# Performance work log

Measured on AMD Instinct MI355X. Metric: run time of the kernel, lower is better.

Reference implementation:

```python
import jax, jax.numpy as jnp
import numpy as np
from jax.scipy.special import logsumexp

WORD_DIM = 512
SCRF_DIM = 256
N_TAGS = 12
ALLOWED_SPAN = 8
START_ID = 10
STOP_ID = 11
SEQ_LEN = 768
N_SPANS = 96


def _compute_scores(h, Wl, bl, Wr, br, Gl, bgl, Gr, bgr, Wt, bt, transitions):
    # h: [1, L, D] already projected by Dense
    Lc, D = h.shape[1], h.shape[2]
    scores = jnp.zeros((1, Lc, Lc, D), h.dtype)
    diag = jnp.arange(Lc)
    ht = h
    scores = scores.at[:, diag, diag].set(ht)
    for sl in range(1, min(ALLOWED_SPAN, Lc)):
        l, r = ht[:, :-1], ht[:, 1:]
        h_hat = 4.0 * jax.nn.sigmoid(l @ Wl.T + bl + r @ Wr.T + br) - 2.0
        # exp/normalize over 3 gates == softmax over gate axis
        g = (l @ Gl.T + bgl + r @ Gr.T + bgr).reshape(1, Lc - sl, 3, D)
        wgt = jax.nn.softmax(g, axis=2)
        ht = wgt[:, :, 0] * h_hat + wgt[:, :, 1] * l + wgt[:, :, 2] * r
        scores = scores.at[:, diag[:Lc - sl], diag[sl:]].set(ht)
    tagsc = scores @ Wt.T + bt  # [1, L, L, T]
    # final[b,i,j,prev,tag] = tagsc[b,i,j,tag] + transitions[prev,tag]
    return tagsc[:, :, :, None, :] + transitions[None, None, None]


def _forward_pass(s5):
    # s5: [1, L, L, T, T]; semi-Markov forward algorithm, windows of width <= ALLOWED_SPAN
    Lc, T = s5.shape[1], s5.shape[3]
    A = ALLOWED_SPAN
    i0 = jnp.arange(1, Lc + 1)
    k = jnp.arange(A)
    p = i0[:, None] - A + k[None, :]              # candidate span-start positions [L, A]
    m = p >= 0                                    # valid window mask (istarts = max(0, i-A))
    x = s5[0][jnp.clip(p, 0), (i0 - 1)[:, None]]  # [L, A, T, T] span scores ending at i-1
    buf0 = jnp.full((A, T), -10000.0, s5.dtype).at[A - 1, START_ID].set(0.0)

    def step(buf, inp):
        xi, mi = inp
        # tmp[k, prev, tag] = score + logalpha[start, prev]
        tmp = jnp.where(mi[:, None, None], xi + buf[:, :, None], -1e30)
        na = logsumexp(tmp, axis=(0, 1))  # [T]
        return jnp.concatenate([buf[1:], na[None]], axis=0), na

    _, alphas = jax.lax.scan(step, buf0, (x, m))
    return alphas[-1, :STOP_ID].sum()


def _gold_score(s5, tags):
    Lc, T = s5.shape[1], s5.shape[3]
    gf = tags[:, :, 0] * (Lc * T * T) + tags[:, :, 1] * (T * T) + tags[:, :, 2] * T + tags[:, :, 3]
    return jnp.take_along_axis(s5.reshape(1, -1), gf, axis=1).sum()


def setup_inputs() -> dict:
    key = jax.random.key(0)
    ks = jax.random.split(key, 16)
    D, W3 = SCRF_DIM, 3 * SCRF_DIM
    s = 0.05
    def w(k, shape):
        return jax.random.normal(k, shape, dtype=jnp.float32) * s
    return {
        "feats": jax.random.normal(ks[0], (1, SEQ_LEN, WORD_DIM), dtype=jnp.float32),
        "tags": jax.random.randint(ks[1], (1, N_SPANS, 4), 0, N_TAGS),
        "Wd": w(ks[2], (D, WORD_DIM)), "bd": jnp.zeros((D,), jnp.float32),
        "Wl": w(ks[3], (D, D)), "bl": jnp.zeros((D,), jnp.float32),
        "Wr": w(ks[4], (D, D)), "br": jnp.zeros((D,), jnp.float32),
        "Gl": w(ks[5], (W3, D)), "bgl": jnp.zeros((W3,), jnp.float32),
        "Gr": w(ks[6], (W3, D)), "bgr": jnp.zeros((W3,), jnp.float32),
        "Wt": w(ks[7], (N_TAGS, D)), "bt": jnp.zeros((N_TAGS,), jnp.float32),
        "transitions": w(ks[8], (N_TAGS, N_TAGS)),
    }


def reference(feats, tags, Wd, bd, Wl, bl, Wr, br, Gl, bgl, Gr, bgr, Wt, bt, transitions):
    h = feats @ Wd.T + bd  # Dense: word_dim -> scrf_dim
    s5 = _compute_scores(h, Wl, bl, Wr, br, Gl, bgl, Gr, bgr, Wt, bt, transitions)
    gold = _gold_score(s5, tags)
    logZ = _forward_pass(s5)
    return logZ - gold
```

## Files before the change

kernel.cpp:

```cpp
#include <hip/hip_runtime.h>

typedef __attribute__((ext_vector_type(8))) short short8;
typedef __attribute__((ext_vector_type(4))) float f32x4;

#define TPAD 100

__device__ __forceinline__ float bf2f(short s) {
  return __uint_as_float(((unsigned)(unsigned short)s) << 16);
}
__device__ __forceinline__ unsigned short f2bf(float f) {
  unsigned u = __float_as_uint(f);
  unsigned rounding = 0x7fffu + ((u >> 16) & 1u);
  return (unsigned short)((u + rounding) >> 16);
}

__device__ __forceinline__ void stg_f32(float* p, float v) {
  asm volatile("global_store_dword %0, %1, off sc1" :: "v"(p), "v"(v) : "memory");
}
__device__ __forceinline__ void stg_u16(unsigned short* p, unsigned short v) {
  unsigned w = v;
  asm volatile("global_store_short %0, %1, off sc1" :: "v"(p), "v"(w) : "memory");
}
__device__ __forceinline__ void stg_u32(unsigned* p, unsigned v) {
  asm volatile("global_store_dword %0, %1, off sc1" :: "v"(p), "v"(v) : "memory");
}

#define NFLAGS 18432
__device__ __forceinline__ void flag_spin(unsigned* f, unsigned tgt) {
  unsigned n = 0;
  while (__hip_atomic_load(f, __ATOMIC_RELAXED, __HIP_MEMORY_SCOPE_AGENT) < tgt) {
    __builtin_amdgcn_s_sleep(1);
    if (++n > 2000000u) break;
  }
}
#define DRAIN() asm volatile("s_waitcnt vmcnt(0) lgkmcnt(0)" ::: "memory")

union __align__(16) SmemU {
  struct { unsigned short As[64][72]; unsigned short Ws[64][72]; float Cs[64][64]; } g;
  struct { unsigned short rows[2][8][264]; float sred[2][96]; float smu[2]; } bn;
  struct { float Bs[96 * TPAD]; float Acs[96 * TPAD]; float red[8]; } t;
  struct { float Qs[2][96 * TPAD]; float vv[4][96]; float red[8]; float redm[4]; } f;
};

__global__ void prep_kernel(const float* __restrict__ feats, const float* __restrict__ Wd,
                            const float* __restrict__ Wl, const float* __restrict__ Wr,
                            const float* __restrict__ Gl, const float* __restrict__ Gr,
                            const float* __restrict__ bl, const float* __restrict__ br,
                            const float* __restrict__ bgl, const float* __restrict__ bgr,
                            unsigned short* __restrict__ featsB, unsigned short* __restrict__ WdB,
                            unsigned short* __restrict__ WcB, float* __restrict__ bc,
                            unsigned* __restrict__ flags)
{
  int idx = blockIdx.x * 256 + threadIdx.x;
  if (idx < 393216) {
    featsB[idx] = f2bf(feats[idx]);
  } else if (idx < 524288) {
    int j = idx - 393216;
    WdB[j] = f2bf(Wd[j]);
  } else if (idx < 1048576) {
    int j = idx - 524288;
    int o = j >> 9, k = j & 511;
    float v;
    if (k < 256) v = (o < 256) ? Wl[o*256 + k] : Gl[(o-256)*256 + k];
    else { int k2 = k - 256; v = (o < 256) ? Wr[o*256 + k2] : Gr[(o-256)*256 + k2]; }
    WcB[j] = f2bf(v);
  } else if (idx < 1049600) {
    int o = idx - 1048576;
    bc[o] = (o < 256) ? bl[o] + br[o] : bgl[o-256] + bgr[o-256];
  } else {
    int j = idx - 1049600;
    if (j < NFLAGS) flags[j] = 0u;
  }
}

__device__ __forceinline__ void treelevel(SmemU& sm,
    const float* Tin, const float* Cin, float* Tout, float* Cout)
{
  const int bid = blockIdx.x;
  const int tid = threadIdx.x;
  const int wv = tid >> 6, lane = tid & 63;
  const int j = bid >> 1;
  const int cs = (bid & 1) * 48;
  const float* Ag = Tin + (size_t)(2*j) * 9216;
  const float* Bg = Tin + (size_t)(2*j + 1) * 9216;

  float4 av[9], bv[9];
  const float* ap = Ag + tid * 36;
  const float* bp = Bg + tid * 36;
  #pragma unroll
  for (int q = 0; q < 9; ++q) av[q] = *(const float4*)(ap + q*4);
  #pragma unroll
  for (int q = 0; q < 9; ++q) bv[q] = *(const float4*)(bp + q*4);
  float ma = 0.f, mb = 0.f;
  #pragma unroll
  for (int q = 0; q < 9; ++q) {
    ma = fmaxf(ma, fmaxf(fmaxf(av[q].x, av[q].y), fmaxf(av[q].z, av[q].w)));
    mb = fmaxf(mb, fmaxf(fmaxf(bv[q].x, bv[q].y), fmaxf(bv[q].z, bv[q].w)));
  }
  #pragma unroll
  for (int off = 32; off; off >>= 1) {
    ma = fmaxf(ma, __shfl_down(ma, off));
    mb = fmaxf(mb, __shfl_down(mb, off));
  }
  if (lane == 0) { sm.t.red[wv] = ma; sm.t.red[4 + wv] = mb; }
  __syncthreads();
  float fa = fmaxf(fmaxf(sm.t.red[0], sm.t.red[1]), fmaxf(sm.t.red[2], sm.t.red[3]));
  float fb = fmaxf(fmaxf(sm.t.red[4], sm.t.red[5]), fmaxf(sm.t.red[6], sm.t.red[7]));
  float ia = 1.0f / fa, ib = 1.0f / fb;

  #pragma unroll
  for (int q = 0; q < 9; ++q) {
    int e = tid*36 + q*4;
    int r = e / 96, k = e - r*96;
    float4 bb = bv[q];
    bb.x *= ib; bb.y *= ib; bb.z *= ib; bb.w *= ib;
    *(float4*)&sm.t.Bs[r*TPAD + k] = bb;
    float4 aa = av[q];
    sm.t.Acs[(k+0)*TPAD + r] = aa.x * ia;
    sm.t.Acs[(k+1)*TPAD + r] = aa.y * ia;
    sm.t.Acs[(k+2)*TPAD + r] = aa.z * ia;
    sm.t.Acs[(k+3)*TPAD + r] = aa.w * ia;
  }
  __syncthreads();

  int tr = tid >> 4, tc = tid & 15;
  int r0 = tr * 6, c0 = cs + tc * 3;
  float acc[6][3];
  #pragma unroll
  for (int i = 0; i < 6; ++i)
    #pragma unroll
    for (int m = 0; m < 3; ++m) acc[i][m] = 0.f;
  for (int k = 0; k < 96; k += 4) {
    float4 a0 = *(const float4*)&sm.t.Acs[(c0+0)*TPAD + k];
    float4 a1 = *(const float4*)&sm.t.Acs[(c0+1)*TPAD + k];
    float4 a2 = *(const float4*)&sm.t.Acs[(c0+2)*TPAD + k];
    #pragma unroll
    for (int i = 0; i < 6; ++i) {
      float4 b = *(const float4*)&sm.t.Bs[(r0+i)*TPAD + k];
      acc[i][0] += b.x*a0.x + b.y*a0.y + b.z*a0.z + b.w*a0.w;
      acc[i][1] += b.x*a1.x + b.y*a1.y + b.z*a1.z + b.w*a1.w;
      acc[i][2] += b.x*a2.x + b.y*a2.y + b.z*a2.z + b.w*a2.w;
    }
  }
  float* op = Tout + (size_t)j * 9216;
  #pragma unroll
  for (int i = 0; i < 6; ++i)
    #pragma unroll
    for (int m = 0; m < 3; ++m)
      stg_f32(&op[(size_t)(r0+i)*96 + c0 + m], acc[i][m]);
  if ((bid & 1) == 0 && tid == 0)
    stg_f32(&Cout[j], Cin[2*j] + Cin[2*j + 1] + __logf(fa) + __logf(fb));
}

__global__ __launch_bounds__(256, 2) void mega_kernel(
    const unsigned short* featsB, const unsigned short* WdB,
    const float* bd, const unsigned short* WcB, const float* bc,
    unsigned short* ht, const float* Wt, const float* bt,
    float* Bband, float* Xn, float* muv, const float* trans,
    const int* tags,
    float* T0, float* T1, float* T2, float* T3, float* T4,
    float* C0, float* C1, float* C2, float* C3, float* C4,
    float* out, unsigned* flags)
{
  __shared__ SmemU sm;
  const int bid = blockIdx.x;
  const int tid = threadIdx.x;
  const int wave = tid >> 6, lane = tid & 63;

  if (bid < 192) {
    const int p = bid % 12;
    const int lr = tid >> 3;
    const int c8 = (tid & 7) * 8;
    if (bid < 48) {
      const int p0 = p * 64;
      const int n0 = (bid / 12) * 64;
      f32x4 acc[4];
      #pragma unroll
      for (int i = 0; i < 4; ++i)
        #pragma unroll
        for (int j = 0; j < 4; ++j) acc[i][j] = 0.f;
      short8 a0r, a1r, w0r, w1r;
      a0r = *(const short8*)(featsB + (size_t)(p0 + lr)*512 + c8);
      a1r = *(const short8*)(featsB + (size_t)(p0 + lr + 32)*512 + c8);
      w0r = *(const short8*)(WdB + (size_t)(n0 + lr)*512 + c8);
      w1r = *(const short8*)(WdB + (size_t)(n0 + lr + 32)*512 + c8);
      for (int kt = 0; kt < 8; ++kt) {
        *(short8*)(&sm.g.As[lr][c8])      = a0r;
        *(short8*)(&sm.g.As[lr + 32][c8]) = a1r;
        *(short8*)(&sm.g.Ws[lr][c8])      = w0r;
        *(short8*)(&sm.g.Ws[lr + 32][c8]) = w1r;
        __syncthreads();
        if (kt < 7) {
          int kb = (kt + 1) * 64;
          a0r = *(const short8*)(featsB + (size_t)(p0 + lr)*512 + kb + c8);
          a1r = *(const short8*)(featsB + (size_t)(p0 + lr + 32)*512 + kb + c8);
          w0r = *(const short8*)(WdB + (size_t)(n0 + lr)*512 + kb + c8);
          w1r = *(const short8*)(WdB + (size_t)(n0 + lr + 32)*512 + kb + c8);
        }
        int q8 = (lane >> 4) * 8;
        #pragma unroll
        for (int kk = 0; kk < 2; ++kk) {
          short8 bfr = *(const short8*)(&sm.g.Ws[wave*16 + (lane & 15)][kk*32 + q8]);
          #pragma unroll
          for (int mt = 0; mt < 4; ++mt) {
            short8 afr = *(const short8*)(&sm.g.As[mt*16 + (lane & 15)][kk*32 + q8]);
            acc[mt] = __builtin_amdgcn_mfma_f32_16x16x32_bf16(afr, bfr, acc[mt], 0, 0, 0);
          }
        }
        __syncthreads();
      }
      int o = n0 + wave*16 + (lane & 15);
      float bias = bd[o];
      #pragma unroll
      for (int mt = 0; mt < 4; ++mt)
        #pragma unroll
        for (int r = 0; r < 4; ++r) {
          int row = p0 + mt*16 + (lane >> 4)*4 + r;
          stg_u16(&ht[row*256 + o], f2bf(acc[mt][r] + bias));
        }
      DRAIN();
      __syncthreads();
      if (tid == 0) atomicAdd(&flags[(0*12 + p)*32], 1u);
    }

    const int p0 = p * 64;
    const int n0i = (bid / 12) * 16;
    for (int sl = 1; sl <= 7; ++sl) {
      short8 w0r, w1r, a0r, a1r;
      {
        int o0 = (lr >> 4)*256 + n0i + (lr & 15);
        int o1 = ((lr+32) >> 4)*256 + n0i + ((lr+32) & 15);
        w0r = *(const short8*)(WcB + (size_t)o0*512 + c8);
        w1r = *(const short8*)(WcB + (size_t)o1*512 + c8);
      }
      unsigned tgt = (sl == 1) ? 4u : 16u;
      if (tid == 0) {
        flag_spin(&flags[((sl-1)*12 + p)*32], tgt);
        if (p < 11) flag_spin(&flags[((sl-1)*12 + p + 1)*32], tgt);
      }
      __syncthreads();
      {
        const unsigned short* htp = ht + (size_t)(sl - 1) * 196608;
        unsigned short* htn = ht + (size_t)sl * 196608;
        const int Mvalid = 768 - sl;
        f32x4 acc[4];
        #pragma unroll
        for (int i = 0; i < 4; ++i)
          #pragma unroll
          for (int j = 0; j < 4; ++j) acc[i][j] = 0.f;
        {
          int g0 = p0 + lr;      if (g0 > 767) g0 = 767;
          int g1 = p0 + lr + 32; if (g1 > 767) g1 = 767;
          a0r = *(const short8*)(htp + (size_t)g0*256 + c8);
          a1r = *(const short8*)(htp + (size_t)g1*256 + c8);
        }
        for (int kt = 0; kt < 8; ++kt) {
          *(short8*)(&sm.g.As[lr][c8])      = a0r;
          *(short8*)(&sm.g.As[lr + 32][c8]) = a1r;
          *(short8*)(&sm.g.Ws[lr][c8])      = w0r;
          *(short8*)(&sm.g.Ws[lr + 32][c8]) = w1r;
          __syncthreads();
          if (kt < 7) {
            int kb = (kt + 1) * 64;
            int shift = kb >> 8;
            int kcol = kb & 255;
            int g0 = p0 + lr + shift;      if (g0 > 767) g0 = 767;
            int g1 = p0 + lr + 32 + shift; if (g1 > 767) g1 = 767;
            a0r = *(const short8*)(htp + (size_t)g0*256 + kcol + c8);
            a1r = *(const short8*)(htp + (size_t)g1*256 + kcol + c8);
            int o0 = (lr >> 4)*256 + n0i + (lr & 15);
            int o1 = ((lr+32) >> 4)*256 + n0i + ((lr+32) & 15);
            w0r = *(const short8*)(WcB + (size_t)o0*512 + kb + c8);
            w1r = *(const short8*)(WcB + (size_t)o1*512 + kb + c8);
          }
          int q8 = (lane >> 4) * 8;
          #pragma unroll
          for (int kk = 0; kk < 2; ++kk) {
            short8 bfr = *(const short8*)(&sm.g.Ws[wave*16 + (lane & 15)][kk*32 + q8]);
            #pragma unroll
            for (int mt = 0; mt < 4; ++mt) {
              short8 afr = *(const short8*)(&sm.g.As[mt*16 + (lane & 15)][kk*32 + q8]);
              acc[mt] = __builtin_amdgcn_mfma_f32_16x16x32_bf16(afr, bfr, acc[mt], 0, 0, 0);
            }
          }
          __syncthreads();
        }
        #pragma unroll
        for (int mt = 0; mt < 4; ++mt)
          #pragma unroll
          for (int r = 0; r < 4; ++r)
            sm.g.Cs[mt*16 + (lane >> 4)*4 + r][wave*16 + (lane & 15)] = acc[mt][r];
        __syncthreads();

        int dl = tid & 7;
        int d0 = n0i + dl*2;
        int cc0 = dl*2;
        float bz0 = bc[d0],       bz1 = bc[d0+1];
        float b00 = bc[256 + d0], b01 = bc[256 + d0 + 1];
        float b10 = bc[512 + d0], b11 = bc[512 + d0 + 1];
        float b20 = bc[768 + d0], b21 = bc[768 + d0 + 1];
        for (int pr = tid >> 3; pr < 64; pr += 32) {
          int pw = p0 + pr;
          if (pw >= Mvalid) continue;
          float z0 = sm.g.Cs[pr][cc0]      + bz0, z1 = sm.g.Cs[pr][cc0+1]      + bz1;
          float g00 = sm.g.Cs[pr][16+cc0]  + b00, g01 = sm.g.Cs[pr][16+cc0+1]  + b01;
          float g10 = sm.g.Cs[pr][32+cc0]  + b10, g11 = sm.g.Cs[pr][32+cc0+1]  + b11;
          float g20 = sm.g.Cs[pr][48+cc0]  + b20, g21 = sm.g.Cs[pr][48+cc0+1]  + b21;
          unsigned lv = *(const unsigned*)(htp + (size_t)pw*256 + d0);
          unsigned rv = *(const unsigned*)(htp + (size_t)(pw+1)*256 + d0);
          float l0 = bf2f((short)(lv & 0xffff)), l1 = bf2f((short)(lv >> 16));
          float r0v = bf2f((short)(rv & 0xffff)), r1v = bf2f((short)(rv >> 16));
          float hh0 = 4.f / (1.f + __expf(-z0)) - 2.f;
          float hh1 = 4.f / (1.f + __expf(-z1)) - 2.f;
          float mg0 = fmaxf(g00, fmaxf(g10, g20));
          float mg1 = fmaxf(g01, fmaxf(g11, g21));
          float e00 = __expf(g00 - mg0), e10 = __expf(g10 - mg0), e20 = __expf(g20 - mg0);
          float e01 = __expf(g01 - mg1), e11 = __expf(g11 - mg1), e21 = __expf(g21 - mg1);
          float o0 = (e00*hh0 + e10*l0 + e20*r0v) / (e00 + e10 + e20);
          float o1 = (e01*hh1 + e11*l1 + e21*r1v) / (e01 + e11 + e21);
          unsigned pack = (unsigned)f2bf(o0) | ((unsigned)f2bf(o1) << 16);
          stg_u32((unsigned*)(htn + (size_t)pw*256 + d0), pack);
        }
      }
      DRAIN();
      __syncthreads();
      if (tid == 0) atomicAdd(&flags[(sl*12 + p)*32], 1u);
    }
  }

  for (int task = bid; task < 384; task += 256) {
    if (tid == 0) {
      int rlo = 2*task - 7; if (rlo < 0) rlo = 0;
      int tlo = rlo >> 6, thi = (2*task + 1) >> 6;
      flag_spin(&flags[(7*12 + tlo)*32], 16u);
      if (thi != tlo) flag_spin(&flags[(7*12 + thi)*32], 16u);
    }
    __syncthreads();
    const int half = tid >> 7;
    const int t2 = tid & 127;
    const int i = 2*task + 1 + half;
    for (int q = t2; q < 256; q += 128) {
      int k = q >> 5, cc = (q & 31) * 8;
      int pr = i - 8 + k;
      short8 v;
      if (pr >= 0) {
        int slx = 7 - k;
        v = *(const short8*)(ht + ((size_t)slx*768 + pr)*256 + cc);
      } else {
        #pragma unroll
        for (int j = 0; j < 8; ++j) v[j] = 0;
      }
      *(short8*)(&sm.bn.rows[half][k][cc]) = v;
    }
    __syncthreads();
    float res = -1e30f;
    if (t2 < 96) {
      int t = t2 >> 3, k = t2 & 7;
      int pr = i - 8 + k;
      if (pr >= 0) {
        float acc = 0.f;
        for (int dch = 0; dch < 256; dch += 8) {
          float4 wa = *(const float4*)(Wt + t*256 + dch);
          float4 wb = *(const float4*)(Wt + t*256 + dch + 4);
          short8 hv = *(const short8*)(&sm.bn.rows[half][k][dch]);
          acc += wa.x*bf2f(hv[0]) + wa.y*bf2f(hv[1]) + wa.z*bf2f(hv[2]) + wa.w*bf2f(hv[3])
               + wb.x*bf2f(hv[4]) + wb.y*bf2f(hv[5]) + wb.z*bf2f(hv[6]) + wb.w*bf2f(hv[7]);
        }
        res = acc + bt[t];
      }
      stg_f32(&Bband[(size_t)i*96 + t2], res);
      sm.bn.sred[half][t2] = res;
    }
    __syncthreads();
    if (t2 < 32) {
      float m = fmaxf(sm.bn.sred[half][t2],
                 fmaxf(sm.bn.sred[half][t2+32], sm.bn.sred[half][t2+64]));
      #pragma unroll
      for (int off = 16; off; off >>= 1) m = fmaxf(m, __shfl_down(m, off));
      if (t2 == 0) { stg_f32(&muv[i], m); sm.bn.smu[half] = m; }
    }
    __syncthreads();
    if (t2 < 96) stg_f32(&Xn[(size_t)i*96 + t2], __expf(res - sm.bn.smu[half]));
    DRAIN();
    __syncthreads();
    if (tid == 0) atomicAdd(&flags[(96 + task)*32], 1u);
  }
  if (bid >= 240) return;

  {
    const int chunk = bid / 5;
    const int bxx = bid % 5;
    if (tid == 0) {
      #pragma unroll
      for (int q = 0; q < 8; ++q)
        flag_spin(&flags[(96 + 8*chunk + q)*32], 1u);
    }
    __syncthreads();
    if (bxx == 0 && tid == 0) stg_f32(&C0[chunk], 0.f);
    const int a = chunk * 16;
    const int g = lane / 12;
    const int t = lane - g * 12;
    const int cidx = bxx * 20 + wave * 5 + g;
    const bool active = (g < 5) && (cidx < 96);
    const int c = active ? cidx : 95;
    const int s = c / 12, tau = c - s * 12;
    float Etc[12];
    #pragma unroll
    for (int jj = 0; jj < 12; ++jj) Etc[jj] = __expf(trans[jj*12 + t]);
    float NA[8], V[8];
    #pragma unroll
    for (int jj = 0; jj < 8; ++jj) { NA[jj] = 0.f; V[jj] = 0.f; }
    #pragma unroll
    for (int jj = 0; jj < 8; ++jj) if (jj == s) {
      NA[jj] = (t == tau) ? 1.f : 0.f;
      V[jj]  = Etc[tau];
    }
    const int gbb = (g * 12) * 4;
    #pragma unroll
    for (int m = 1; m <= 16; ++m) {
      const float* xr = Xn + (size_t)(a + m) * 96 + t * 8;
      float4 x0 = *(const float4*)xr;
      float4 x1 = *(const float4*)(xr + 4);
      float sf = __expf(-muv[a + m]);
      float na = x0.x*V[0] + x0.y*V[1] + x0.z*V[2] + x0.w*V[3]
               + x1.x*V[4] + x1.y*V[5] + x1.z*V[6] + x1.w*V[7];
      int nai = __float_as_int(na);
      float nb[12];
      #pragma unroll
      for (int jj = 0; jj < 12; ++jj)
        nb[jj] = __int_as_float(__builtin_amdgcn_ds_bpermute(gbb + jj*4, nai));
      float pp0 = nb[0]*Etc[0] + nb[1]*Etc[1] + nb[2]*Etc[2]   + nb[3]*Etc[3];
      float pp1 = nb[4]*Etc[4] + nb[5]*Etc[5] + nb[6]*Etc[6]   + nb[7]*Etc[7];
      float pp2 = nb[8]*Etc[8] + nb[9]*Etc[9] + nb[10]*Etc[10] + nb[11]*Etc[11];
      float v = (pp0 + pp1) + pp2;
      #pragma unroll
      for (int kq = 0; kq < 7; ++kq) { NA[kq] = NA[kq+1]*sf; V[kq] = V[kq+1]*sf; }
      NA[7] = na; V[7] = v;
    }
    if (active) {
      float* dst = T0 + (size_t)chunk * 9216 + c;
      #pragma unroll
      for (int jj = 0; jj < 8; ++jj) stg_f32(&dst[(size_t)(jj*12 + t) * 96], NA[jj]);
    }
    DRAIN();
    __syncthreads();
    if (tid == 0) atomicAdd(&flags[(480 + chunk)*32], 1u);
  }
  if (bid >= 48) return;

  {
    int j = bid >> 1;
    if (tid == 0) {
      flag_spin(&flags[(480 + 2*j    )*32], 5u);
      flag_spin(&flags[(480 + 2*j + 1)*32], 5u);
    }
    __syncthreads();
    treelevel(sm, T0, C0, T1, C1);
    DRAIN(); __syncthreads();
    if (tid == 0) atomicAdd(&flags[(528 + j)*32], 1u);
  }
  if (bid >= 24) return;
  {
    int j = bid >> 1;
    if (tid == 0) {
      flag_spin(&flags[(528 + 2*j    )*32], 2u);
      flag_spin(&flags[(528 + 2*j + 1)*32], 2u);
    }
    __syncthreads();
    treelevel(sm, T1, C1, T2, C2);
    DRAIN(); __syncthreads();
    if (tid == 0) atomicAdd(&flags[(552 + j)*32], 1u);
  }
  if (bid >= 12) return;
  {
    int j = bid >> 1;
    if (tid == 0) {
      flag_spin(&flags[(552 + 2*j    )*32], 2u);
      flag_spin(&flags[(552 + 2*j + 1)*32], 2u);
    }
    __syncthreads();
    treelevel(sm, T2, C2, T3, C3);
    DRAIN(); __syncthreads();
    if (tid == 0) atomicAdd(&flags[(564 + j)*32], 1u);
  }
  if (bid >= 6) return;
  {
    int j = bid >> 1;
    if (tid == 0) {
      flag_spin(&flags[(564 + 2*j    )*32], 2u);
      flag_spin(&flags[(564 + 2*j + 1)*32], 2u);
    }
    __syncthreads();
    treelevel(sm, T3, C3, T4, C4);
    DRAIN(); __syncthreads();
    if (tid == 0) atomicAdd(&flags[(570 + j)*32], 1u);
  }
  if (bid) return;

  {
    if (tid == 0) {
      flag_spin(&flags[(570)*32], 2u);
      flag_spin(&flags[(571)*32], 2u);
      flag_spin(&flags[(572)*32], 2u);
    }
    __syncthreads();
    float4 P[9];
    const float* p0p = T4 + tid * 36;
    #pragma unroll
    for (int q = 0; q < 9; ++q) P[q] = *(const float4*)(p0p + q*4);

    float gold = 0.f;
    if (tid < 96) {
      int a = tags[tid*4+0], b = tags[tid*4+1], cc = tags[tid*4+2], d = tags[tid*4+3];
      float v = trans[cc*12 + d];
      int sl = b - a;
      if (sl >= 0 && sl < 8) v += Bband[(size_t)(b+1)*96 + d*8 + (7 - sl)];
      else v += bt[d];
      gold = v;
    }
    float mp = 0.f;
    for (int q = tid; q < 768; q += 256) mp += muv[1 + q];
    #pragma unroll
    for (int off = 32; off; off >>= 1) {
      gold += __shfl_down(gold, off);
      mp   += __shfl_down(mp, off);
    }
    if (lane == 0) { sm.f.red[wave] = gold; sm.f.red[4 + wave] = mp; }

    #pragma unroll
    for (int q = 0; q < 9; ++q) {
      int e = tid*36 + q*4;
      int r = e / 96, k = e - r*96;
      *(float4*)&sm.f.Qs[0][r*TPAD + k] = P[q];
    }
    if (tid < 96) sm.f.vv[0][tid] = (tid == 94) ? 1.f : 0.f;
    __syncthreads();
    float gold_t = sm.f.red[0] + sm.f.red[1] + sm.f.red[2] + sm.f.red[3];
    float musum  = sm.f.red[4] + sm.f.red[5] + sm.f.red[6] + sm.f.red[7];
    float Ct = C4[0] + C4[1] + C4[2];

    #pragma unroll
    for (int s = 0; s < 3; ++s) {
      if (s < 2) {
        const float* pn = T4 + (size_t)(s+1)*9216 + tid*36;
        #pragma unroll
        for (int q = 0; q < 9; ++q) P[q] = *(const float4*)(pn + q*4);
      }
      float acc = 0.f;
      if (tid < 96) {
        const float* Qr = &sm.f.Qs[s & 1][tid * TPAD];
        #pragma unroll
        for (int k = 0; k < 96; k += 4) {
          float4 qv = *(const float4*)(Qr + k);
          float4 zv = *(const float4*)&sm.f.vv[s][k];
          acc += qv.x*zv.x + qv.y*zv.y + qv.z*zv.z + qv.w*zv.w;
        }
      }
      float am = (tid < 96) ? acc : 0.f;
      #pragma unroll
      for (int off = 32; off; off >>= 1) am = fmaxf(am, __shfl_down(am, off));
      if (lane == 0) sm.f.redm[wave] = am;
      __syncthreads();
      float mx = fmaxf(fmaxf(sm.f.redm[0], sm.f.redm[1]), fmaxf(sm.f.redm[2], sm.f.redm[3]));
      Ct += __logf(mx);
      if (tid < 96) sm.f.vv[s+1][tid] = acc / mx;
      if (s < 2) {
        #pragma unroll
        for (int q = 0; q < 9; ++q) {
          int e = tid*36 + q*4;
          int r = e / 96, k = e - r*96;
          *(float4*)&sm.f.Qs[(s+1)&1][r*TPAD + k] = P[q];
        }
      }
      __syncthreads();
    }
    if (tid == 0) {
      float lsum = 0.f;
      #pragma unroll
      for (int t = 0; t < 11; ++t) lsum += __logf(sm.f.vv[3][84 + t]);
      out[0] = lsum + 11.f * (Ct + musum) - gold_t;
    }
  }
}

extern "C" void kernel_launch(void* const* d_in, const int* in_sizes, int n_in,
                              void* d_out, int out_size, void* d_ws, size_t ws_size,
                              hipStream_t stream)
{
  const float* feats = (const float*)d_in[0];
  const int*   tags  = (const int*)  d_in[1];
  const float* Wd    = (const float*)d_in[2];
  const float* bd    = (const float*)d_in[3];
  const float* Wl    = (const float*)d_in[4];
  const float* bl    = (const float*)d_in[5];
  const float* Wr    = (const float*)d_in[6];
  const float* br    = (const float*)d_in[7];
  const float* Gl    = (const float*)d_in[8];
  const float* bgl   = (const float*)d_in[9];
  const float* Gr    = (const float*)d_in[10];
  const float* bgr   = (const float*)d_in[11];
  const float* Wt    = (const float*)d_in[12];
  const float* bt    = (const float*)d_in[13];
  const float* trans = (const float*)d_in[14];
  float* out = (float*)d_out;

  char* ws = (char*)d_ws;
  unsigned short* featsB = (unsigned short*)(ws + 0);
  unsigned short* WdB    = (unsigned short*)(ws + 786432);
  unsigned short* WcB    = (unsigned short*)(ws + 1048576);
  float*          bc     = (float*)         (ws + 2097152);
  unsigned short* ht     = (unsigned short*)(ws + 2101248);
  float*          Bband  = (float*)         (ws + 5246976);
  float*          Xn     = (float*)         (ws + 5542272);
  float*          muv    = (float*)         (ws + 5837568);
  float*          T0     = (float*)         (ws + 5841664);
  float*          T1     = (float*)         (ws + 7611136);
  float*          T2     = (float*)         (ws + 8495872);
  float*          T3     = (float*)         (ws + 8938240);
  float*          T4     = (float*)         (ws + 9159424);
  float*          C0     = (float*)         (ws + 9270016);
  float*          C1     = (float*)         (ws + 9270272);
  float*          C2     = (float*)         (ws + 9270528);
  float*          C3     = (float*)         (ws + 9270784);
  float*          C4     = (float*)         (ws + 9271040);
  unsigned*       flags  = (unsigned*)      (ws + 9271296);

  prep_kernel<<<4172, 256, 0, stream>>>(feats, Wd, Wl, Wr, Gl, Gr, bl, br, bgl, bgr,
                                        featsB, WdB, WcB, bc, flags);
  mega_kernel<<<256, 256, 0, stream>>>(featsB, WdB, bd, WcB, bc, ht, Wt, bt,
                                       Bband, Xn, muv, trans, tags,
                                       T0, T1, T2, T3, T4, C0, C1, C2, C3, C4,
                                       out, flags);
}
```

Baseline: 211.6 us.

## Fuse bf16 conversion into mega kernel and double-buffer GEMM LDS tiles

Drops the feats/Wd bf16 pre-conversion from the prep kernel: the projection GEMM now loads fp32 inputs and converts them in registers, and blocks 48+ build the combined WcB weight inside the mega kernel, with a flag that the span GEMMs wait on. Both GEMM loops get double-buffered LDS tiles, a two-stage register prefetch, and a lighter barrier macro. This removes most of the prep kernel's work and one global round trip, and overlaps loads with MFMA. In exchange it adds a new cross-block dependency through a spin flag, doubles the LDS tile footprint, and lowers launch bounds to one block per CU.

```diff
diff --git a/kernel.cpp b/kernel.cpp
--- a/kernel.cpp
+++ b/kernel.cpp
@@ -12,6 +12,17 @@
   unsigned u = __float_as_uint(f);
   unsigned rounding = 0x7fffu + ((u >> 16) & 1u);
   return (unsigned short)((u + rounding) >> 16);
+}
+
+struct F8 { float4 a, b; };
+__device__ __forceinline__ F8 ldf8(const float* p) {
+  F8 r; r.a = *(const float4*)p; r.b = *(const float4*)(p + 4); return r;
+}
+__device__ __forceinline__ short8 cvtF8(F8 v) {
+  short8 r;
+  r[0]=(short)f2bf(v.a.x); r[1]=(short)f2bf(v.a.y); r[2]=(short)f2bf(v.a.z); r[3]=(short)f2bf(v.a.w);
+  r[4]=(short)f2bf(v.b.x); r[5]=(short)f2bf(v.b.y); r[6]=(short)f2bf(v.b.z); r[7]=(short)f2bf(v.b.w);
+  return r;
 }
 
 __device__ __forceinline__ void stg_f32(float* p, float v) {
@@ -34,41 +45,28 @@
   }
 }
 #define DRAIN() asm volatile("s_waitcnt vmcnt(0) lgkmcnt(0)" ::: "memory")
+#define KTBAR() do { \
+  asm volatile("s_waitcnt lgkmcnt(0)" ::: "memory"); \
+  __builtin_amdgcn_s_barrier(); \
+  __builtin_amdgcn_sched_barrier(0); \
+} while (0)
 
 union __align__(16) SmemU {
-  struct { unsigned short As[64][72]; unsigned short Ws[64][72]; float Cs[64][64]; } g;
+  struct { unsigned short As[2][64][72]; unsigned short Ws[2][64][72]; float Cs[64][64]; } g;
   struct { unsigned short rows[2][8][264]; float sred[2][96]; float smu[2]; } bn;
   struct { float Bs[96 * TPAD]; float Acs[96 * TPAD]; float red[8]; } t;
   struct { float Qs[2][96 * TPAD]; float vv[4][96]; float red[8]; float redm[4]; } f;
 };
 
-__global__ void prep_kernel(const float* __restrict__ feats, const float* __restrict__ Wd,
-                            const float* __restrict__ Wl, const float* __restrict__ Wr,
-                            const float* __restrict__ Gl, const float* __restrict__ Gr,
-                            const float* __restrict__ bl, const float* __restrict__ br,
+__global__ void prep_kernel(const float* __restrict__ bl, const float* __restrict__ br,
                             const float* __restrict__ bgl, const float* __restrict__ bgr,
-                            unsigned short* __restrict__ featsB, unsigned short* __restrict__ WdB,
-                            unsigned short* __restrict__ WcB, float* __restrict__ bc,
-                            unsigned* __restrict__ flags)
+                            float* __restrict__ bc, unsigned* __restrict__ flags)
 {
   int idx = blockIdx.x * 256 + threadIdx.x;
-  if (idx < 393216) {
-    featsB[idx] = f2bf(feats[idx]);
-  } else if (idx < 524288) {
-    int j = idx - 393216;
-    WdB[j] = f2bf(Wd[j]);
-  } else if (idx < 1048576) {
-    int j = idx - 524288;
-    int o = j >> 9, k = j & 511;
-    float v;
-    if (k < 256) v = (o < 256) ? Wl[o*256 + k] : Gl[(o-256)*256 + k];
-    else { int k2 = k - 256; v = (o < 256) ? Wr[o*256 + k2] : Gr[(o-256)*256 + k2]; }
-    WcB[j] = f2bf(v);
-  } else if (idx < 1049600) {
-    int o = idx - 1048576;
-    bc[o] = (o < 256) ? bl[o] + br[o] : bgl[o-256] + bgr[o-256];
+  if (idx < 1024) {
+    bc[idx] = (idx < 256) ? bl[idx] + br[idx] : bgl[idx-256] + bgr[idx-256];
   } else {
-    int j = idx - 1049600;
+    int j = idx - 1024;
     if (j < NFLAGS) flags[j] = 0u;
   }
 }
@@ -152,9 +150,10 @@
     stg_f32(&Cout[j], Cin[2*j] + Cin[2*j + 1] + __logf(fa) + __logf(fb));
 }
 
-__global__ __launch_bounds__(256, 2) void mega_kernel(
-    const unsigned short* featsB, const unsigned short* WdB,
-    const float* bd, const unsigned short* WcB, const float* bc,
+__global__ __launch_bounds__(256, 1) void mega_kernel(
+    const float* feats, const float* Wd, const float* bd,
+    const float* Wl, const float* Wr, const float* Gl, const float* Gr,
+    unsigned short* WcB, const float* bc,
     unsigned short* ht, const float* Wt, const float* bt,
     float* Bband, float* Xn, float* muv, const float* trans,
     const int* tags,
@@ -167,6 +166,19 @@
   const int tid = threadIdx.x;
   const int wave = tid >> 6, lane = tid & 63;
 
+  if (bid >= 48) {
+    for (int j = (bid - 48)*256 + tid; j < 524288; j += 208*256) {
+      int o = j >> 9, k = j & 511;
+      float v;
+      if (k < 256) v = (o < 256) ? Wl[o*256 + k] : Gl[(o-256)*256 + k];
+      else { int k2 = k - 256; v = (o < 256) ? Wr[o*256 + k2] : Gr[(o-256)*256 + k2]; }
+      stg_u16(&WcB[j], f2bf(v));
+    }
+    DRAIN();
+    __syncthreads();
+    if (tid == 0) atomicAdd(&flags[573*32], 1u);
+  }
+
   if (bid < 192) {
     const int p = bid % 12;
     const int lr = tid >> 3;
@@ -179,35 +191,41 @@
       for (int i = 0; i < 4; ++i)
         #pragma unroll
         for (int j = 0; j < 4; ++j) acc[i][j] = 0.f;
-      short8 a0r, a1r, w0r, w1r;
-      a0r = *(const short8*)(featsB + (size_t)(p0 + lr)*512 + c8);
-      a1r = *(const short8*)(featsB + (size_t)(p0 + lr + 32)*512 + c8);
-      w0r = *(const short8*)(WdB + (size_t)(n0 + lr)*512 + c8);
-      w1r = *(const short8*)(WdB + (size_t)(n0 + lr + 32)*512 + c8);
+      F8 fa0[2], fa1[2], fw0[2], fw1[2];
+      #pragma unroll
+      for (int q = 0; q < 2; ++q) {
+        int kb = q * 64;
+        fa0[q] = ldf8(feats + (size_t)(p0 + lr)*512 + kb + c8);
+        fa1[q] = ldf8(feats + (size_t)(p0 + lr + 32)*512 + kb + c8);
+        fw0[q] = ldf8(Wd + (size_t)(n0 + lr)*512 + kb + c8);
+        fw1[q] = ldf8(Wd + (size_t)(n0 + lr + 32)*512 + kb + c8);
+      }
+      #pragma unroll
       for (int kt = 0; kt < 8; ++kt) {
-        *(short8*)(&sm.g.As[lr][c8])      = a0r;
-        *(short8*)(&sm.g.As[lr + 32][c8]) = a1r;
-        *(short8*)(&sm.g.Ws[lr][c8])      = w0r;
-        *(short8*)(&sm.g.Ws[lr + 32][c8]) = w1r;
-        __syncthreads();
-        if (kt < 7) {
-          int kb = (kt + 1) * 64;
-          a0r = *(const short8*)(featsB + (size_t)(p0 + lr)*512 + kb + c8);
-          a1r = *(const short8*)(featsB + (size_t)(p0 + lr + 32)*512 + kb + c8);
-          w0r = *(const short8*)(WdB + (size_t)(n0 + lr)*512 + kb + c8);
-          w1r = *(const short8*)(WdB + (size_t)(n0 + lr + 32)*512 + kb + c8);
-        }
+        const int sb = kt & 1;
+        *(short8*)(&sm.g.As[sb][lr][c8])      = cvtF8(fa0[sb]);
+        *(short8*)(&sm.g.As[sb][lr + 32][c8]) = cvtF8(fa1[sb]);
+        *(short8*)(&sm.g.Ws[sb][lr][c8])      = cvtF8(fw0[sb]);
+        *(short8*)(&sm.g.Ws[sb][lr + 32][c8]) = cvtF8(fw1[sb]);
+        if (kt < 6) {
+          int kb = (kt + 2) * 64;
+          fa0[sb] = ldf8(feats + (size_t)(p0 + lr)*512 + kb + c8);
+          fa1[sb] = ldf8(feats + (size_t)(p0 + lr + 32)*512 + kb + c8);
+          fw0[sb] = ldf8(Wd + (size_t)(n0 + lr)*512 + kb + c8);
+          fw1[sb] = ldf8(Wd + (size_t)(n0 + lr + 32)*512 + kb + c8);
+        }
+        KTBAR();
         int q8 = (lane >> 4) * 8;
         #pragma unroll
         for (int kk = 0; kk < 2; ++kk) {
-          short8 bfr = *(const short8*)(&sm.g.Ws[wave*16 + (lane & 15)][kk*32 + q8]);
+          short8 bfr = *(const short8*)(&sm.g.Ws[sb][wave*16 + (lane & 15)][kk*32 + q8]);
           #pragma unroll
           for (int mt = 0; mt < 4; ++mt) {
-            short8 afr = *(const short8*)(&sm.g.As[mt*16 + (lane & 15)][kk*32 + q8]);
+            short8 afr = *(const short8*)(&sm.g.As[sb][mt*16 + (lane & 15)][kk*32 + q8]);
             acc[mt] = __builtin_amdgcn_mfma_f32_16x16x32_bf16(afr, bfr, acc[mt], 0, 0, 0);
           }
         }
-        __syncthreads();
+        KTBAR();
       }
       int o = n0 + wave*16 + (lane & 15);
       float bias = bd[o];
@@ -225,13 +243,19 @@
 
     const int p0 = p * 64;
     const int n0i = (bid / 12) * 16;
+    const int o0w = (lr >> 4)*256 + n0i + (lr & 15);
+    const int o1w = ((lr+32) >> 4)*256 + n0i + ((lr+32) & 15);
     for (int sl = 1; sl <= 7; ++sl) {
-      short8 w0r, w1r, a0r, a1r;
-      {
-        int o0 = (lr >> 4)*256 + n0i + (lr & 15);
-        int o1 = ((lr+32) >> 4)*256 + n0i + ((lr+32) & 15);
-        w0r = *(const short8*)(WcB + (size_t)o0*512 + c8);
-        w1r = *(const short8*)(WcB + (size_t)o1*512 + c8);
+      if (sl == 1) {
+        if (tid == 0) flag_spin(&flags[573*32], 208u);
+        __syncthreads();
+      }
+      short8 sw0[2], sw1[2], sa0[2], sa1[2];
+      #pragma unroll
+      for (int q = 0; q < 2; ++q) {
+        int kb = q * 64;
+        sw0[q] = *(const short8*)(WcB + (size_t)o0w*512 + kb + c8);
+        sw1[q] = *(const short8*)(WcB + (size_t)o1w*512 + kb + c8);
       }
       unsigned tgt = (sl == 1) ? 4u : 16u;
       if (tid == 0) {
@@ -248,42 +272,44 @@
         for (int i = 0; i < 4; ++i)
           #pragma unroll
           for (int j = 0; j < 4; ++j) acc[i][j] = 0.f;
-        {
+        #pragma unroll
+        for (int q = 0; q < 2; ++q) {
+          int kb = q * 64;
           int g0 = p0 + lr;      if (g0 > 767) g0 = 767;
           int g1 = p0 + lr + 32; if (g1 > 767) g1 = 767;
-          a0r = *(const short8*)(htp + (size_t)g0*256 + c8);
-          a1r = *(const short8*)(htp + (size_t)g1*256 + c8);
-        }
+          sa0[q] = *(const short8*)(htp + (size_t)g0*256 + kb + c8);
+          sa1[q] = *(const short8*)(htp + (size_t)g1*256 + kb + c8);
+        }
+        #pragma unroll
         for (int kt = 0; kt < 8; ++kt) {
-          *(short8*)(&sm.g.As[lr][c8])      = a0r;
-          *(short8*)(&sm.g.As[lr + 32][c8]) = a1r;
-          *(short8*)(&sm.g.Ws[lr][c8])      = w0r;
-          *(short8*)(&sm.g.Ws[lr + 32][c8]) = w1r;
-          __syncthreads();
-          if (kt < 7) {
-            int kb = (kt + 1) * 64;
+          const int sb = kt & 1;
+          *(short8*)(&sm.g.As[sb][lr][c8])      = sa0[sb];
+          *(short8*)(&sm.g.As[sb][lr + 32][c8]) = sa1[sb];
+          *(short8*)(&sm.g.Ws[sb][lr][c8])      = sw0[sb];
+          *(short8*)(&sm.g.Ws[sb][lr + 32][c8]) = sw1[sb];
+          if (kt < 6) {
+            int kb = (kt + 2) * 64;
             int shift = kb >> 8;
             int kcol = kb & 255;
             int g0 = p0 + lr + shift;      if (g0 > 767) g0 = 767;
             int g1 = p0 + lr + 32 + shift; if (g1 > 767) g1 = 767;
-            a0r = *(const short8*)(htp + (size_t)g0*256 + kcol + c8);
-            a1r = *(const short8*)(htp + (size_t)g1*256 + kcol + c8);
-            int o0 = (lr >> 4)*256 + n0i + (lr & 15);
-            int o1 = ((lr+32) >> 4)*256 + n0i + ((lr+32) & 15);
-            w0r = *(const short8*)(WcB + (size_t)o0*512 + kb + c8);
-            w1r = *(const short8*)(WcB + (size_t)o1*512 + kb + c8);
+            sa0[sb] = *(const short8*)(htp + (size_t)g0*256 + kcol + c8);
+            sa1[sb] = *(const short8*)(htp + (size_t)g1*256 + kcol + c8);
+            sw0[sb] = *(const short8*)(WcB + (size_t)o0w*512 + kb + c8);
+            sw1[sb] = *(const short8*)(WcB + (size_t)o1w*512 + kb + c8);
           }
+          KTBAR();
           int q8 = (lane >> 4) * 8;
           #pragma unroll
           for (int kk = 0; kk < 2; ++kk) {
-            short8 bfr = *(const short8*)(&sm.g.Ws[wave*16 + (lane & 15)][kk*32 + q8]);
+            short8 bfr = *(const short8*)(&sm.g.Ws[sb][wave*16 + (lane & 15)][kk*32 + q8]);
             #pragma unroll
             for (int mt = 0; mt < 4; ++mt) {
-              short8 afr = *(const short8*)(&sm.g.As[mt*16 + (lane & 15)][kk*32 + q8]);
+              short8 afr = *(const short8*)(&sm.g.As[sb][mt*16 + (lane & 15)][kk*32 + q8]);
               acc[mt] = __builtin_amdgcn_mfma_f32_16x16x32_bf16(afr, bfr, acc[mt], 0, 0, 0);
             }
           }
-          __syncthreads();
+          KTBAR();
         }
         #pragma unroll
         for (int mt = 0; mt < 4; ++mt)
@@ -605,8 +631,6 @@
   float* out = (float*)d_out;
 
   char* ws = (char*)d_ws;
-  unsigned short* featsB = (unsigned short*)(ws + 0);
-  unsigned short* WdB    = (unsigned short*)(ws + 786432);
   unsigned short* WcB    = (unsigned short*)(ws + 1048576);
   float*          bc     = (float*)         (ws + 2097152);
   unsigned short* ht     = (unsigned short*)(ws + 2101248);
@@ -625,10 +649,9 @@
   float*          C4     = (float*)         (ws + 9271040);
   unsigned*       flags  = (unsigned*)      (ws + 9271296);
 
-  prep_kernel<<<4172, 256, 0, stream>>>(feats, Wd, Wl, Wr, Gl, Gr, bl, br, bgl, bgr,
-                                        featsB, WdB, WcB, bc, flags);
-  mega_kernel<<<256, 256, 0, stream>>>(featsB, WdB, bd, WcB, bc, ht, Wt, bt,
-                                       Bband, Xn, muv, trans, tags,
+  prep_kernel<<<76, 256, 0, stream>>>(bl, br, bgl, bgr, bc, flags);
+  mega_kernel<<<256, 256, 0, stream>>>(feats, Wd, bd, Wl, Wr, Gl, Gr, WcB, bc,
+                                       ht, Wt, bt, Bband, Xn, muv, trans, tags,
                                        T0, T1, T2, T3, T4, C0, C1, C2, C3, C4,
                                        out, flags);
 }
```

Result: faster. 204.1 us (-3.5%).
